# Kernel tuning notes

Hardware: AMD Instinct MI355X
Metric: run time of the kernel (lower is better)

Reference implementation:

```python
import jax, jax.numpy as jnp
import numpy as np

DIM = 2048
NUM_HEADS = 16
HEAD_DIM = DIM // NUM_HEADS
ROPE_BASE = 10000.0


def _rope_cos_sin(seq_len, head_dim, dtype):
    inv_freq = 1.0 / (ROPE_BASE ** (jnp.arange(0, head_dim, 2, dtype=jnp.float32) / head_dim))
    t = jnp.arange(seq_len, dtype=jnp.float32)
    freqs = jnp.einsum('i,j->ij', t, inv_freq)            # (T, head_dim/2)
    emb = jnp.concatenate([freqs, freqs], axis=-1)        # (T, head_dim)
    return jnp.cos(emb).astype(dtype), jnp.sin(emb).astype(dtype)


def _rotate_half(x):
    x1, x2 = jnp.split(x, 2, axis=-1)
    return jnp.concatenate([-x2, x1], axis=-1)


def setup_inputs() -> dict:
    key = jax.random.key(0)
    k1, k2, k3 = jax.random.split(key, 3)
    B, T = 2, 2048
    x = jax.random.normal(k1, (B, T, DIM), dtype=jnp.float32)
    # scale weights like nn.Linear default init (~1/sqrt(fan_in))
    w_qkv = jax.random.normal(k2, (DIM, 3 * DIM), dtype=jnp.float32) / np.sqrt(DIM)
    w_out = jax.random.normal(k3, (DIM, DIM), dtype=jnp.float32) / np.sqrt(DIM)
    return {"x": x, "w_qkv": w_qkv, "w_out": w_out}


def reference(x, w_qkv, w_out):
    B, T, D = x.shape
    H, Hd = NUM_HEADS, HEAD_DIM
    scale = Hd ** -0.5

    qkv = x @ w_qkv                                        # (B, T, 3D)
    q, k, v = jnp.split(qkv, 3, axis=-1)
    # (B, H, T, Hd)
    q = q.reshape(B, T, H, Hd).transpose(0, 2, 1, 3)
    k = k.reshape(B, T, H, Hd).transpose(0, 2, 1, 3)
    v = v.reshape(B, T, H, Hd).transpose(0, 2, 1, 3)

    cos, sin = _rope_cos_sin(T, Hd, x.dtype)               # (T, Hd)
    q = q * cos + _rotate_half(q) * sin
    k = k * cos + _rotate_half(k) * sin

    scores = jnp.einsum('bhqd,bhkd->bhqk', q, k) * scale   # (B, H, T, T)
    causal = jnp.tril(jnp.ones((T, T), dtype=bool))
    scores = jnp.where(causal[None, None, :, :], scores, jnp.float32(-jnp.inf))
    attn = jax.nn.softmax(scores, axis=-1)

    out = jnp.einsum('bhqk,bhkd->bhqd', attn, v)           # (B, H, T, Hd)
    out = out.transpose(0, 2, 1, 3).reshape(B, T, D)
    return out @ w_out
```

## Files before the change

kernel.cpp:

```cpp
#include <hip/hip_runtime.h>

typedef __attribute__((ext_vector_type(8))) short bf16x8;
typedef __attribute__((ext_vector_type(4))) float f32x4;

#define DEVICE __device__ __forceinline__

static constexpr int Tc = 2048;
static constexpr int Dc = 2048;
static constexpr int Hc = 16;
static constexpr int HD = 128;
static constexpr int MR = 4096;
static constexpr int NQKV = 6144;

DEVICE float bf2f(unsigned short u) {
  unsigned int t = ((unsigned int)u) << 16;
  float f; __builtin_memcpy(&f, &t, 4); return f;
}
DEVICE unsigned short f2bf(float f) {
  unsigned int t; __builtin_memcpy(&t, &f, 4);
  unsigned int r = (t + 0x7fffu + ((t >> 16) & 1u)) >> 16;
  return (unsigned short)r;
}

DEVICE void async_cp16(const void* g, void* lds) {
  __builtin_amdgcn_global_load_lds((const __attribute__((address_space(1))) void*)g,
                                   (__attribute__((address_space(3))) void*)lds, 16, 0, 0);
}

DEVICE int lsw(int t, int d2) {
  return t * 256 + (d2 ^ ((((t & 7) ^ ((t >> 3) & 7)) << 4)));
}

__global__ void rope_table_kernel(float2* cs) {
  int t = blockIdx.x;
  int j = threadIdx.x;
  float inv = powf(10000.0f, -(float)(2 * j) / 128.0f);
  float ang = (float)t * inv;
  cs[t * 64 + j] = make_float2(cosf(ang), sinf(ang));
}

__global__ void f32_to_bf16_kernel(const float* __restrict__ in,
                                   unsigned short* __restrict__ out, int n) {
  int i = (blockIdx.x * blockDim.x + threadIdx.x) * 4;
  if (i >= n) return;
  float4 v = *(const float4*)(in + i);
  ushort4 o;
  o.x = f2bf(v.x); o.y = f2bf(v.y); o.z = f2bf(v.z); o.w = f2bf(v.w);
  *(ushort4*)(out + i) = o;
}

__global__ __launch_bounds__(256)
void transpose_f32_bf16_kernel(const float* __restrict__ in,
                               unsigned short* __restrict__ out,
                               int R, int C) {
  __shared__ float tile[64][68];
  int c0 = blockIdx.x * 64, r0 = blockIdx.y * 64;
  int tid = threadIdx.x;
#pragma unroll
  for (int it = 0; it < 4; ++it) {
    int idx = it * 256 + tid;
    int r = idx >> 4;
    int c = (idx & 15) * 4;
    float4 v = *(const float4*)&in[(size_t)(r0 + r) * C + c0 + c];
    tile[r][c] = v.x; tile[r][c + 1] = v.y;
    tile[r][c + 2] = v.z; tile[r][c + 3] = v.w;
  }
  __syncthreads();
#pragma unroll
  for (int it = 0; it < 2; ++it) {
    int idx = it * 256 + tid;
    int r = idx >> 3;
    int c = (idx & 7) * 8;
    bf16x8 ov;
#pragma unroll
    for (int i = 0; i < 8; ++i) ov[i] = (short)f2bf(tile[c + i][r]);
    *(bf16x8*)&out[(size_t)(c0 + r) * R + r0 + c] = ov;
  }
}

__global__ __launch_bounds__(256, 2)
void gemm_qkv_kernel(const unsigned short* __restrict__ A,
                     const unsigned short* __restrict__ Bt,
                     const float2* __restrict__ cs,
                     unsigned short* __restrict__ qh,
                     unsigned short* __restrict__ kh,
                     unsigned short* __restrict__ vt) {
  const int N = NQKV, K = Dc;
  __shared__ __align__(16) unsigned short sh[128 * 128];
  unsigned short* As = sh;
  unsigned short* Bs = sh + 128 * 64;

  int nbx = N >> 7;
  int nwg = gridDim.x;
  int wg = blockIdx.x;
  int cpx = nwg >> 3;
  wg = (wg & 7) * cpx + (wg >> 3);
  int gsize = nbx * 8;
  int g = wg / gsize, rem = wg - g * gsize;
  int by = g * 8 + (rem & 7), bx = rem >> 3;
  int m0 = by << 7, n0 = bx << 7;

  int tid = threadIdx.x, lane = tid & 63, wid = tid >> 6;
  int wm = (wid >> 1) << 6, wn = (wid & 1) << 6;

  f32x4 acc[4][4] = {};

  for (int k0 = 0; k0 < K; k0 += 64) {
    __syncthreads();
#pragma unroll
    for (int r = 0; r < 4; ++r) {
      int p = r * 4096 + wid * 1024 + lane * 16;
      int row = p >> 7;
      int cb = (p & 127) ^ ((row & 7) << 4);
      const char* ga = (const char*)A + ((size_t)(m0 + row) * K + k0) * 2 + cb;
      async_cp16(ga, (char*)As + r * 4096 + wid * 1024);
      const char* gb = (const char*)Bt + ((size_t)(n0 + row) * K + k0) * 2 + cb;
      async_cp16(gb, (char*)Bs + r * 4096 + wid * 1024);
    }
    __syncthreads();

#pragma unroll
    for (int ks = 0; ks < 2; ++ks) {
      bf16x8 af[4], bfr[4];
#pragma unroll
      for (int mi = 0; mi < 4; ++mi) {
        int row = wm + mi * 16 + (lane & 15);
        int cb = (ks * 64 + ((lane >> 4) << 4)) ^ ((row & 7) << 4);
        af[mi] = *(const bf16x8*)((const char*)As + row * 128 + cb);
      }
#pragma unroll
      for (int ni = 0; ni < 4; ++ni) {
        int row = wn + ni * 16 + (lane & 15);
        int cb = (ks * 64 + ((lane >> 4) << 4)) ^ ((row & 7) << 4);
        bfr[ni] = *(const bf16x8*)((const char*)Bs + row * 128 + cb);
      }
#pragma unroll
      for (int mi = 0; mi < 4; ++mi)
#pragma unroll
        for (int ni = 0; ni < 4; ++ni)
          acc[mi][ni] = __builtin_amdgcn_mfma_f32_16x16x32_bf16(
              af[mi], bfr[ni], acc[mi][ni], 0, 0, 0);
    }
  }

  __syncthreads();
#pragma unroll
  for (int mi = 0; mi < 4; ++mi)
#pragma unroll
    for (int ni = 0; ni < 4; ++ni)
#pragma unroll
      for (int r = 0; r < 4; ++r) {
        int t_ = wm + mi * 16 + ((lane >> 4) << 2) + r;
        int d_ = wn + ni * 16 + (lane & 15);
        *(unsigned short*)((char*)sh + lsw(t_, d_ * 2)) = f2bf(acc[mi][ni][r]);
      }
  __syncthreads();

  int sector = n0 >> 11;
  int h = (n0 & 2047) >> 7;
  if (sector < 2) {
    unsigned short* dst = sector ? kh : qh;
#pragma unroll
    for (int it = 0; it < 4; ++it) {
      int idx = it * 256 + tid;
      int r = idx >> 3, j0 = (idx & 7) * 8;
      int m = m0 + r;
      int t = m & (Tc - 1), b = m >> 11;
      bf16x8 o1, o2;
#pragma unroll
      for (int i = 0; i < 8; ++i) {
        float q1 = bf2f(*(const unsigned short*)((const char*)sh + lsw(r, (j0 + i) * 2)));
        float q2 = bf2f(*(const unsigned short*)((const char*)sh + lsw(r, (j0 + i + 64) * 2)));
        float2 c = cs[t * 64 + j0 + i];
        o1[i] = (short)f2bf(q1 * c.x - q2 * c.y);
        o2[i] = (short)f2bf(q2 * c.x + q1 * c.y);
      }
      size_t ob = ((size_t)(b * Hc + h) * Tc + t) * HD;
      *(bf16x8*)(dst + ob + j0) = o1;
      *(bf16x8*)(dst + ob + 64 + j0) = o2;
    }
  } else {
    int bh = (m0 >> 11) * Hc + h;
    int tb = m0 & (Tc - 1);
#pragma unroll
    for (int it = 0; it < 8; ++it) {
      int idx = it * 256 + tid;
      int d = idx >> 4, tc = idx & 15;
      bf16x8 o;
#pragma unroll
      for (int i = 0; i < 8; ++i)
        o[i] = (short)*(const unsigned short*)((const char*)sh + lsw(tc * 8 + i, d * 2));
      *(bf16x8*)(vt + (size_t)(bh * HD + d) * Tc + tb + tc * 8) = o;
    }
  }
}

__global__ __launch_bounds__(256, 2)
void gemm_bt_kernel(const unsigned short* __restrict__ A,
                    const unsigned short* __restrict__ Bt,
                    float* __restrict__ C, int M, int N, int K) {
  __shared__ unsigned short As[128 * 64];
  __shared__ unsigned short Bs[128 * 64];

  int nbx = N >> 7;
  int nwg = gridDim.x;
  int wg = blockIdx.x;
  int cpx = nwg >> 3;
  wg = (wg & 7) * cpx + (wg >> 3);
  int gsize = nbx * 8;
  int g = wg / gsize, rem = wg - g * gsize;
  int by = g * 8 + (rem & 7), bx = rem >> 3;
  int m0 = by << 7, n0 = bx << 7;

  int tid = threadIdx.x, lane = tid & 63, wid = tid >> 6;
  int wm = (wid >> 1) << 6, wn = (wid & 1) << 6;

  f32x4 acc[4][4] = {};

  for (int k0 = 0; k0 < K; k0 += 64) {
    __syncthreads();
#pragma unroll
    for (int r = 0; r < 4; ++r) {
      int p = r * 4096 + wid * 1024 + lane * 16;
      int row = p >> 7;
      int cb = (p & 127) ^ ((row & 7) << 4);
      const char* ga = (const char*)A + ((size_t)(m0 + row) * K + k0) * 2 + cb;
      async_cp16(ga, (char*)As + r * 4096 + wid * 1024);
      const char* gb = (const char*)Bt + ((size_t)(n0 + row) * K + k0) * 2 + cb;
      async_cp16(gb, (char*)Bs + r * 4096 + wid * 1024);
    }
    __syncthreads();

#pragma unroll
    for (int ks = 0; ks < 2; ++ks) {
      bf16x8 af[4], bfr[4];
#pragma unroll
      for (int mi = 0; mi < 4; ++mi) {
        int row = wm + mi * 16 + (lane & 15);
        int cb = (ks * 64 + ((lane >> 4) << 4)) ^ ((row & 7) << 4);
        af[mi] = *(const bf16x8*)((const char*)As + row * 128 + cb);
      }
#pragma unroll
      for (int ni = 0; ni < 4; ++ni) {
        int row = wn + ni * 16 + (lane & 15);
        int cb = (ks * 64 + ((lane >> 4) << 4)) ^ ((row & 7) << 4);
        bfr[ni] = *(const bf16x8*)((const char*)Bs + row * 128 + cb);
      }
#pragma unroll
      for (int mi = 0; mi < 4; ++mi)
#pragma unroll
        for (int ni = 0; ni < 4; ++ni)
          acc[mi][ni] = __builtin_amdgcn_mfma_f32_16x16x32_bf16(
              af[mi], bfr[ni], acc[mi][ni], 0, 0, 0);
    }
  }

#pragma unroll
  for (int mi = 0; mi < 4; ++mi)
#pragma unroll
    for (int ni = 0; ni < 4; ++ni)
#pragma unroll
      for (int r = 0; r < 4; ++r) {
        int row = m0 + wm + mi * 16 + ((lane >> 4) << 2) + r;
        int col = n0 + wn + ni * 16 + (lane & 15);
        C[(size_t)row * N + col] = acc[mi][ni][r];
      }
}

__global__ __launch_bounds__(512, 1)
void attn_kernel(const unsigned short* __restrict__ qh,
                 const unsigned short* __restrict__ kh,
                 const unsigned short* __restrict__ vt,
                 unsigned short* __restrict__ ao) {
  const float SCL2 = 0.08838834764831845f * 1.4426950408889634f;
  int bh = blockIdx.x;
  int pairp = blockIdx.y;
  int b = bh >> 4, h = bh & 15;

  __shared__ unsigned short Ks[3][64 * 128];
  __shared__ unsigned short Vs[3][128 * 64];
  __shared__ unsigned short Ps[8][16 * 64];

  int tid = threadIdx.x, lane = tid & 63, wid = tid >> 6;

  const unsigned short* Kg = kh + (size_t)bh * Tc * HD;
  const unsigned short* Vg = vt + (size_t)bh * HD * Tc;

  auto stage = [&](int kt, int buf) {
#pragma unroll
    for (int r = 0; r < 2; ++r) {
      int p = r * 8192 + wid * 1024 + lane * 16;
      {
        int row = p >> 8, cb = p & 255;
        const char* g = (const char*)Kg + ((size_t)(kt * 64 + row)) * 256 +
                        (cb ^ ((row & 7) << 4));
        async_cp16(g, (char*)&Ks[buf][0] + r * 8192 + wid * 1024);
      }
      {
        int d = p >> 7, cb = p & 127;
        const char* g = (const char*)Vg + (size_t)d * (Tc * 2) + kt * 128 +
                        (cb ^ ((d & 7) << 4));
        async_cp16(g, (char*)&Vs[buf][0] + r * 8192 + wid * 1024);
      }
    }
  };

#pragma unroll 1
  for (int pass = 0; pass < 2; ++pass) {
    int qt = pass ? (15 - pairp) : pairp;
    const unsigned short* Qg = qh + ((size_t)bh * Tc + qt * 128) * HD;

    bf16x8 qf[4];
#pragma unroll
    for (int ks = 0; ks < 4; ++ks) {
      int row = wid * 16 + (lane & 15);
      qf[ks] = *(const bf16x8*)((const char*)Qg + row * 256 + ks * 64 +
                                ((lane >> 4) << 4));
    }
    asm volatile("s_waitcnt vmcnt(0)" ::: "memory");

    f32x4 oacc[8] = {};
    float mrow[4], lrow[4];
#pragma unroll
    for (int r = 0; r < 4; ++r) { mrow[r] = -1e30f; lrow[r] = 0.f; }

    int nkt = 2 * (qt + 1);
    __syncthreads();
    stage(0, 0);
    stage(1, 1);
#pragma unroll 1
    for (int kt = 0; kt < nkt; ++kt) {
      if (kt + 1 < nkt)
        asm volatile("s_waitcnt vmcnt(4)" ::: "memory");
      else
        asm volatile("s_waitcnt vmcnt(0)" ::: "memory");
      asm volatile("s_barrier" ::: "memory");
      if (kt + 2 < nkt) stage(kt + 2, (kt + 2) % 3);
      int cur = kt % 3;

      f32x4 sacc[4] = {};
      __builtin_amdgcn_s_setprio(1);
#pragma unroll
      for (int ks = 0; ks < 4; ++ks) {
#pragma unroll
        for (int ni = 0; ni < 4; ++ni) {
          int row = ni * 16 + (lane & 15);
          int cb = (ks * 64 + ((lane >> 4) << 4)) ^ ((row & 7) << 4);
          bf16x8 kf = *(const bf16x8*)((const char*)&Ks[cur][0] + row * 256 + cb);
          sacc[ni] = __builtin_amdgcn_mfma_f32_16x16x32_bf16(qf[ks], kf,
                                                             sacc[ni], 0, 0, 0);
        }
      }
      __builtin_amdgcn_s_setprio(0);

      bool diag = (kt >= 2 * qt);
      float sv[4][4];
      float pmax[4];
      bool allok = true;
#pragma unroll
      for (int r = 0; r < 4; ++r) {
        int qrow = qt * 128 + wid * 16 + ((lane >> 4) << 2) + r;
        float mx = -1e30f;
#pragma unroll
        for (int ni = 0; ni < 4; ++ni) {
          float s = sacc[ni][r] * SCL2;
          if (diag) {
            int kcol = kt * 64 + ni * 16 + (lane & 15);
            if (kcol > qrow) s = -1e30f;
          }
          sv[ni][r] = s;
          mx = fmaxf(mx, s);
        }
        pmax[r] = mx;
        allok = allok && (mx <= mrow[r] + 8.f);
      }
      if (!__all(allok)) {
#pragma unroll
        for (int r = 0; r < 4; ++r) {
          float gm = pmax[r];
          gm = fmaxf(gm, __shfl_xor(gm, 1));
          gm = fmaxf(gm, __shfl_xor(gm, 2));
          gm = fmaxf(gm, __shfl_xor(gm, 4));
          gm = fmaxf(gm, __shfl_xor(gm, 8));
          float mnew = fmaxf(mrow[r], gm);
          float fsc = exp2f(mrow[r] - mnew);
          mrow[r] = mnew;
          lrow[r] *= fsc;
#pragma unroll
          for (int nj = 0; nj < 8; ++nj) oacc[nj][r] *= fsc;
        }
      }

#pragma unroll
      for (int ni = 0; ni < 4; ++ni)
#pragma unroll
        for (int r = 0; r < 4; ++r) {
          float pp = exp2f(sv[ni][r] - mrow[r]);
          lrow[r] += pp;
          int row = ((lane >> 4) << 2) + r;
          int colb = (ni * 16 + (lane & 15)) * 2;
          *(unsigned short*)((char*)&Ps[wid][0] + row * 128 +
                             (colb ^ ((row & 7) << 4))) = f2bf(pp);
        }

      __builtin_amdgcn_s_setprio(1);
#pragma unroll
      for (int ks = 0; ks < 2; ++ks) {
        int prow = lane & 15;
        int pcb = (ks * 64 + ((lane >> 4) << 4)) ^ ((prow & 7) << 4);
        bf16x8 pf = *(const bf16x8*)((const char*)&Ps[wid][0] + prow * 128 + pcb);
#pragma unroll
        for (int nj = 0; nj < 8; ++nj) {
          int vrow = nj * 16 + (lane & 15);
          int vcb = (ks * 64 + ((lane >> 4) << 4)) ^ ((vrow & 7) << 4);
          bf16x8 vf = *(const bf16x8*)((const char*)&Vs[cur][0] + vrow * 128 + vcb);
          oacc[nj] = __builtin_amdgcn_mfma_f32_16x16x32_bf16(pf, vf,
                                                             oacc[nj], 0, 0, 0);
        }
      }
      __builtin_amdgcn_s_setprio(0);
    }

    float inv[4];
#pragma unroll
    for (int r = 0; r < 4; ++r) {
      float s = lrow[r];
      s += __shfl_xor(s, 1);
      s += __shfl_xor(s, 2);
      s += __shfl_xor(s, 4);
      s += __shfl_xor(s, 8);
      inv[r] = 1.f / s;
    }
#pragma unroll
    for (int nj = 0; nj < 8; ++nj)
#pragma unroll
      for (int r = 0; r < 4; ++r) {
        int trow = qt * 128 + wid * 16 + ((lane >> 4) << 2) + r;
        int col = nj * 16 + (lane & 15);
        ao[((size_t)(b * Tc + trow)) * Dc + h * HD + col] =
            f2bf(oacc[nj][r] * inv[r]);
      }
  }
}

extern "C" void kernel_launch(void* const* d_in, const int* in_sizes, int n_in,
                              void* d_out, int out_size, void* d_ws,
                              size_t ws_size, hipStream_t stream) {
  const float* x = (const float*)d_in[0];
  const float* w_qkv = (const float*)d_in[1];
  const float* w_out = (const float*)d_in[2];
  float* out = (float*)d_out;

  char* ws = (char*)d_ws;
  size_t off = 0;
  auto alloc = [&](size_t bytes) {
    char* p = ws + off;
    off += (bytes + 255) & ~(size_t)255;
    return p;
  };
  unsigned short* xb    = (unsigned short*)alloc((size_t)MR * Dc * 2);
  unsigned short* wqkvT = (unsigned short*)alloc((size_t)NQKV * Dc * 2);
  unsigned short* woutT = (unsigned short*)alloc((size_t)Dc * Dc * 2);
  unsigned short* qhp   = (unsigned short*)alloc((size_t)MR * Dc * 2);
  unsigned short* khp   = (unsigned short*)alloc((size_t)MR * Dc * 2);
  unsigned short* vtp   = (unsigned short*)alloc((size_t)MR * Dc * 2);
  unsigned short* aop   = (unsigned short*)alloc((size_t)MR * Dc * 2);
  float2* cs            = (float2*)alloc((size_t)Tc * 64 * sizeof(float2));

  rope_table_kernel<<<Tc, 64, 0, stream>>>(cs);
  f32_to_bf16_kernel<<<(MR * Dc / 4 + 255) / 256, 256, 0, stream>>>(x, xb, MR * Dc);
  transpose_f32_bf16_kernel<<<dim3(NQKV / 64, Dc / 64), 256, 0, stream>>>(
      w_qkv, wqkvT, Dc, NQKV);
  transpose_f32_bf16_kernel<<<dim3(Dc / 64, Dc / 64), 256, 0, stream>>>(
      w_out, woutT, Dc, Dc);
  gemm_qkv_kernel<<<(MR / 128) * (NQKV / 128), 256, 0, stream>>>(
      xb, wqkvT, cs, qhp, khp, vtp);
  attn_kernel<<<dim3(32, 8), 512, 0, stream>>>(qhp, khp, vtp, aop);
  gemm_bt_kernel<<<(MR / 128) * (Dc / 128), 256, 0, stream>>>(
      aop, woutT, out, MR, Dc, Dc);
}
```

Baseline: 250.3 us.

## Halve attention block to 4 waves, each handling 32 query rows

Cuts the attention kernel from 8 to 4 waves per block. Each wave now computes two 16-row query sub-tiles, so every K and V fragment read from LDS feeds two MFMAs instead of one. Staging loops are rewritten so 256 threads cover the same K/V tiles, and the wait count is raised to match the larger number of in-flight copies. This lowers LDS read traffic per MFMA, at the cost of fewer waves to hide latency and roughly double the accumulator registers per thread.

Result: slower. 279.1 us (+11.5%).

```diff
diff --git a/kernel.cpp b/kernel.cpp
--- a/kernel.cpp
+++ b/kernel.cpp
@@ -267,7 +267,7 @@
       }
 }
 
-__global__ __launch_bounds__(512, 1)
+__global__ __launch_bounds__(256, 1)
 void attn_kernel(const unsigned short* __restrict__ qh,
                  const unsigned short* __restrict__ kh,
                  const unsigned short* __restrict__ vt,
@@ -279,7 +279,7 @@
 
   __shared__ unsigned short Ks[3][64 * 128];
   __shared__ unsigned short Vs[3][128 * 64];
-  __shared__ unsigned short Ps[8][16 * 64];
+  __shared__ unsigned short Ps[4][32 * 64];
 
   int tid = threadIdx.x, lane = tid & 63, wid = tid >> 6;
 
@@ -288,19 +288,19 @@
 
   auto stage = [&](int kt, int buf) {
 #pragma unroll
-    for (int r = 0; r < 2; ++r) {
-      int p = r * 8192 + wid * 1024 + lane * 16;
+    for (int r = 0; r < 4; ++r) {
+      int p = r * 4096 + tid * 16;
       {
         int row = p >> 8, cb = p & 255;
         const char* g = (const char*)Kg + ((size_t)(kt * 64 + row)) * 256 +
                         (cb ^ ((row & 7) << 4));
-        async_cp16(g, (char*)&Ks[buf][0] + r * 8192 + wid * 1024);
+        async_cp16(g, (char*)&Ks[buf][0] + (p & ~15));
       }
       {
         int d = p >> 7, cb = p & 127;
         const char* g = (const char*)Vg + (size_t)d * (Tc * 2) + kt * 128 +
                         (cb ^ ((d & 7) << 4));
-        async_cp16(g, (char*)&Vs[buf][0] + r * 8192 + wid * 1024);
+        async_cp16(g, (char*)&Vs[buf][0] + (p & ~15));
       }
     }
   };
@@ -310,19 +310,23 @@
     int qt = pass ? (15 - pairp) : pairp;
     const unsigned short* Qg = qh + ((size_t)bh * Tc + qt * 128) * HD;
 
-    bf16x8 qf[4];
-#pragma unroll
-    for (int ks = 0; ks < 4; ++ks) {
-      int row = wid * 16 + (lane & 15);
-      qf[ks] = *(const bf16x8*)((const char*)Qg + row * 256 + ks * 64 +
-                                ((lane >> 4) << 4));
-    }
+    bf16x8 qf[2][4];
+#pragma unroll
+    for (int mi = 0; mi < 2; ++mi)
+#pragma unroll
+      for (int ks = 0; ks < 4; ++ks) {
+        int row = wid * 32 + mi * 16 + (lane & 15);
+        qf[mi][ks] = *(const bf16x8*)((const char*)Qg + row * 256 + ks * 64 +
+                                      ((lane >> 4) << 4));
+      }
     asm volatile("s_waitcnt vmcnt(0)" ::: "memory");
 
-    f32x4 oacc[8] = {};
-    float mrow[4], lrow[4];
-#pragma unroll
-    for (int r = 0; r < 4; ++r) { mrow[r] = -1e30f; lrow[r] = 0.f; }
+    f32x4 oacc[2][8] = {};
+    float mrow[2][4], lrow[2][4];
+#pragma unroll
+    for (int mi = 0; mi < 2; ++mi)
+#pragma unroll
+      for (int r = 0; r < 4; ++r) { mrow[mi][r] = -1e30f; lrow[mi][r] = 0.f; }
 
     int nkt = 2 * (qt + 1);
     __syncthreads();
@@ -331,14 +335,14 @@
 #pragma unroll 1
     for (int kt = 0; kt < nkt; ++kt) {
       if (kt + 1 < nkt)
-        asm volatile("s_waitcnt vmcnt(4)" ::: "memory");
+        asm volatile("s_waitcnt vmcnt(8)" ::: "memory");
       else
         asm volatile("s_waitcnt vmcnt(0)" ::: "memory");
       asm volatile("s_barrier" ::: "memory");
       if (kt + 2 < nkt) stage(kt + 2, (kt + 2) % 3);
       int cur = kt % 3;
 
-      f32x4 sacc[4] = {};
+      f32x4 sacc[2][4] = {};
       __builtin_amdgcn_s_setprio(1);
 #pragma unroll
       for (int ks = 0; ks < 4; ++ks) {
@@ -347,99 +351,116 @@
           int row = ni * 16 + (lane & 15);
           int cb = (ks * 64 + ((lane >> 4) << 4)) ^ ((row & 7) << 4);
           bf16x8 kf = *(const bf16x8*)((const char*)&Ks[cur][0] + row * 256 + cb);
-          sacc[ni] = __builtin_amdgcn_mfma_f32_16x16x32_bf16(qf[ks], kf,
-                                                             sacc[ni], 0, 0, 0);
+#pragma unroll
+          for (int mi = 0; mi < 2; ++mi)
+            sacc[mi][ni] = __builtin_amdgcn_mfma_f32_16x16x32_bf16(
+                qf[mi][ks], kf, sacc[mi][ni], 0, 0, 0);
         }
       }
       __builtin_amdgcn_s_setprio(0);
 
       bool diag = (kt >= 2 * qt);
-      float sv[4][4];
-      float pmax[4];
+      float sv[2][4][4];
+      float pmax[2][4];
       bool allok = true;
 #pragma unroll
-      for (int r = 0; r < 4; ++r) {
-        int qrow = qt * 128 + wid * 16 + ((lane >> 4) << 2) + r;
-        float mx = -1e30f;
-#pragma unroll
-        for (int ni = 0; ni < 4; ++ni) {
-          float s = sacc[ni][r] * SCL2;
-          if (diag) {
-            int kcol = kt * 64 + ni * 16 + (lane & 15);
-            if (kcol > qrow) s = -1e30f;
+      for (int mi = 0; mi < 2; ++mi)
+#pragma unroll
+        for (int r = 0; r < 4; ++r) {
+          int qrow = qt * 128 + wid * 32 + mi * 16 + ((lane >> 4) << 2) + r;
+          float mx = -1e30f;
+#pragma unroll
+          for (int ni = 0; ni < 4; ++ni) {
+            float s = sacc[mi][ni][r] * SCL2;
+            if (diag) {
+              int kcol = kt * 64 + ni * 16 + (lane & 15);
+              if (kcol > qrow) s = -1e30f;
+            }
+            sv[mi][ni][r] = s;
+            mx = fmaxf(mx, s);
           }
-          sv[ni][r] = s;
-          mx = fmaxf(mx, s);
+          pmax[mi][r] = mx;
+          allok = allok && (mx <= mrow[mi][r] + 8.f);
         }
-        pmax[r] = mx;
-        allok = allok && (mx <= mrow[r] + 8.f);
-      }
       if (!__all(allok)) {
 #pragma unroll
-        for (int r = 0; r < 4; ++r) {
-          float gm = pmax[r];
-          gm = fmaxf(gm, __shfl_xor(gm, 1));
-          gm = fmaxf(gm, __shfl_xor(gm, 2));
-          gm = fmaxf(gm, __shfl_xor(gm, 4));
-          gm = fmaxf(gm, __shfl_xor(gm, 8));
-          float mnew = fmaxf(mrow[r], gm);
-          float fsc = exp2f(mrow[r] - mnew);
-          mrow[r] = mnew;
-          lrow[r] *= fsc;
-#pragma unroll
-          for (int nj = 0; nj < 8; ++nj) oacc[nj][r] *= fsc;
+        for (int mi = 0; mi < 2; ++mi)
+#pragma unroll
+          for (int r = 0; r < 4; ++r) {
+            float gm = pmax[mi][r];
+            gm = fmaxf(gm, __shfl_xor(gm, 1));
+            gm = fmaxf(gm, __shfl_xor(gm, 2));
+            gm = fmaxf(gm, __shfl_xor(gm, 4));
+            gm = fmaxf(gm, __shfl_xor(gm, 8));
+            float mnew = fmaxf(mrow[mi][r], gm);
+            float fsc = exp2f(mrow[mi][r] - mnew);
+            mrow[mi][r] = mnew;
+            lrow[mi][r] *= fsc;
+#pragma unroll
+            for (int nj = 0; nj < 8; ++nj) oacc[mi][nj][r] *= fsc;
+          }
+      }
+
+#pragma unroll
+      for (int mi = 0; mi < 2; ++mi)
+#pragma unroll
+        for (int ni = 0; ni < 4; ++ni)
+#pragma unroll
+          for (int r = 0; r < 4; ++r) {
+            float pp = exp2f(sv[mi][ni][r] - mrow[mi][r]);
+            lrow[mi][r] += pp;
+            int row = mi * 16 + ((lane >> 4) << 2) + r;
+            int colb = (ni * 16 + (lane & 15)) * 2;
+            *(unsigned short*)((char*)&Ps[wid][0] + row * 128 +
+                               (colb ^ ((row & 7) << 4))) = f2bf(pp);
+          }
+
+      __builtin_amdgcn_s_setprio(1);
+#pragma unroll
+      for (int ks = 0; ks < 2; ++ks) {
+        bf16x8 pf[2];
+#pragma unroll
+        for (int mi = 0; mi < 2; ++mi) {
+          int prow = mi * 16 + (lane & 15);
+          int pcb = (ks * 64 + ((lane >> 4) << 4)) ^ ((prow & 7) << 4);
+          pf[mi] = *(const bf16x8*)((const char*)&Ps[wid][0] + prow * 128 + pcb);
         }
-      }
-
-#pragma unroll
-      for (int ni = 0; ni < 4; ++ni)
-#pragma unroll
-        for (int r = 0; r < 4; ++r) {
-          float pp = exp2f(sv[ni][r] - mrow[r]);
-          lrow[r] += pp;
-          int row = ((lane >> 4) << 2) + r;
-          int colb = (ni * 16 + (lane & 15)) * 2;
-          *(unsigned short*)((char*)&Ps[wid][0] + row * 128 +
-                             (colb ^ ((row & 7) << 4))) = f2bf(pp);
-        }
-
-      __builtin_amdgcn_s_setprio(1);
-#pragma unroll
-      for (int ks = 0; ks < 2; ++ks) {
-        int prow = lane & 15;
-        int pcb = (ks * 64 + ((lane >> 4) << 4)) ^ ((prow & 7) << 4);
-        bf16x8 pf = *(const bf16x8*)((const char*)&Ps[wid][0] + prow * 128 + pcb);
 #pragma unroll
         for (int nj = 0; nj < 8; ++nj) {
           int vrow = nj * 16 + (lane & 15);
           int vcb = (ks * 64 + ((lane >> 4) << 4)) ^ ((vrow & 7) << 4);
           bf16x8 vf = *(const bf16x8*)((const char*)&Vs[cur][0] + vrow * 128 + vcb);
-          oacc[nj] = __builtin_amdgcn_mfma_f32_16x16x32_bf16(pf, vf,
-                                                             oacc[nj], 0, 0, 0);
+#pragma unroll
+          for (int mi = 0; mi < 2; ++mi)
+            oacc[mi][nj] = __builtin_amdgcn_mfma_f32_16x16x32_bf16(
+                pf[mi], vf, oacc[mi][nj], 0, 0, 0);
         }
       }
       __builtin_amdgcn_s_setprio(0);
     }
 
-    float inv[4];
-#pragma unroll
-    for (int r = 0; r < 4; ++r) {
-      float s = lrow[r];
-      s += __shfl_xor(s, 1);
-      s += __shfl_xor(s, 2);
-      s += __shfl_xor(s, 4);
-      s += __shfl_xor(s, 8);
-      inv[r] = 1.f / s;
-    }
-#pragma unroll
-    for (int nj = 0; nj < 8; ++nj)
+#pragma unroll
+    for (int mi = 0; mi < 2; ++mi) {
+      float inv[4];
 #pragma unroll
       for (int r = 0; r < 4; ++r) {
-        int trow = qt * 128 + wid * 16 + ((lane >> 4) << 2) + r;
-        int col = nj * 16 + (lane & 15);
-        ao[((size_t)(b * Tc + trow)) * Dc + h * HD + col] =
-            f2bf(oacc[nj][r] * inv[r]);
-      }
+        float s = lrow[mi][r];
+        s += __shfl_xor(s, 1);
+        s += __shfl_xor(s, 2);
+        s += __shfl_xor(s, 4);
+        s += __shfl_xor(s, 8);
+        inv[r] = 1.f / s;
+      }
+#pragma unroll
+      for (int nj = 0; nj < 8; ++nj)
+#pragma unroll
+        for (int r = 0; r < 4; ++r) {
+          int trow = qt * 128 + wid * 32 + mi * 16 + ((lane >> 4) << 2) + r;
+          int col = nj * 16 + (lane & 15);
+          ao[((size_t)(b * Tc + trow)) * Dc + h * HD + col] =
+              f2bf(oacc[mi][nj][r] * inv[r]);
+        }
+    }
   }
 }
 
@@ -475,7 +496,7 @@
       w_out, woutT, Dc, Dc);
   gemm_qkv_kernel<<<(MR / 128) * (NQKV / 128), 256, 0, stream>>>(
       xb, wqkvT, cs, qhp, khp, vtp);
-  attn_kernel<<<dim3(32, 8), 512, 0, stream>>>(qhp, khp, vtp, aop);
+  attn_kernel<<<dim3(32, 8), 256, 0, stream>>>(qhp, khp, vtp, aop);
   gemm_bt_kernel<<<(MR / 128) * (Dc / 128), 256, 0, stream>>>(
       aop, woutT, out, MR, Dc, Dc);
 }
```

## Double-buffer LDS tiles in QKV and output GEMMs to overlap loads with MFMA

Applied to the files above, without the earlier changes.

Both bf16 GEMM kernels now keep two LDS buffers for the A and B tiles and issue the async global-to-LDS copies for the next K tile before computing on the current one. They wait with s_waitcnt vmcnt(8) so only the previous stage's copies must land. The intent is to hide global memory latency behind MFMA work instead of stalling at each barrier. LDS use doubles to 64 KB per block, which may limit occupancy at 2 blocks per CU, and the hand-written waitcnt/barrier sequence depends on the exact count of outstanding loads.

After: 253.3 us. Within noise of the previous version (+1.2%).

```diff
diff --git a/kernel.cpp b/kernel.cpp
--- a/kernel.cpp
+++ b/kernel.cpp
@@ -86,9 +86,7 @@
                      unsigned short* __restrict__ kh,
                      unsigned short* __restrict__ vt) {
   const int N = NQKV, K = Dc;
-  __shared__ __align__(16) unsigned short sh[128 * 128];
-  unsigned short* As = sh;
-  unsigned short* Bs = sh + 128 * 64;
+  __shared__ __align__(16) unsigned short sh[4 * 128 * 64];
 
   int nbx = N >> 7;
   int nwg = gridDim.x;
@@ -105,19 +103,34 @@
 
   f32x4 acc[4][4] = {};
 
-  for (int k0 = 0; k0 < K; k0 += 64) {
-    __syncthreads();
+  auto stage = [&](int kt, int buf) {
+    int k0 = kt << 6;
 #pragma unroll
     for (int r = 0; r < 4; ++r) {
       int p = r * 4096 + wid * 1024 + lane * 16;
       int row = p >> 7;
       int cb = (p & 127) ^ ((row & 7) << 4);
       const char* ga = (const char*)A + ((size_t)(m0 + row) * K + k0) * 2 + cb;
-      async_cp16(ga, (char*)As + r * 4096 + wid * 1024);
+      async_cp16(ga, (char*)(sh + buf * 8192) + r * 4096 + wid * 1024);
       const char* gb = (const char*)Bt + ((size_t)(n0 + row) * K + k0) * 2 + cb;
-      async_cp16(gb, (char*)Bs + r * 4096 + wid * 1024);
-    }
-    __syncthreads();
+      async_cp16(gb, (char*)(sh + 16384 + buf * 8192) + r * 4096 + wid * 1024);
+    }
+  };
+
+  int nkt = K >> 6;
+  stage(0, 0);
+#pragma unroll 1
+  for (int t = 0; t < nkt; ++t) {
+    asm volatile("s_barrier" ::: "memory");
+    if (t + 1 < nkt) {
+      stage(t + 1, (t + 1) & 1);
+      asm volatile("s_waitcnt vmcnt(8)" ::: "memory");
+    } else {
+      asm volatile("s_waitcnt vmcnt(0)" ::: "memory");
+    }
+    asm volatile("s_barrier" ::: "memory");
+    const char* Ab = (const char*)(sh + (t & 1) * 8192);
+    const char* Bb = (const char*)(sh + 16384 + (t & 1) * 8192);
 
 #pragma unroll
     for (int ks = 0; ks < 2; ++ks) {
@@ -126,13 +139,13 @@
       for (int mi = 0; mi < 4; ++mi) {
         int row = wm + mi * 16 + (lane & 15);
         int cb = (ks * 64 + ((lane >> 4) << 4)) ^ ((row & 7) << 4);
-        af[mi] = *(const bf16x8*)((const char*)As + row * 128 + cb);
+        af[mi] = *(const bf16x8*)(Ab + row * 128 + cb);
       }
 #pragma unroll
       for (int ni = 0; ni < 4; ++ni) {
         int row = wn + ni * 16 + (lane & 15);
         int cb = (ks * 64 + ((lane >> 4) << 4)) ^ ((row & 7) << 4);
-        bfr[ni] = *(const bf16x8*)((const char*)Bs + row * 128 + cb);
+        bfr[ni] = *(const bf16x8*)(Bb + row * 128 + cb);
       }
 #pragma unroll
       for (int mi = 0; mi < 4; ++mi)
@@ -199,8 +212,8 @@
 void gemm_bt_kernel(const unsigned short* __restrict__ A,
                     const unsigned short* __restrict__ Bt,
                     float* __restrict__ C, int M, int N, int K) {
-  __shared__ unsigned short As[128 * 64];
-  __shared__ unsigned short Bs[128 * 64];
+  __shared__ __align__(16) unsigned short As[2][128 * 64];
+  __shared__ __align__(16) unsigned short Bs[2][128 * 64];
 
   int nbx = N >> 7;
   int nwg = gridDim.x;
@@ -217,19 +230,34 @@
 
   f32x4 acc[4][4] = {};
 
-  for (int k0 = 0; k0 < K; k0 += 64) {
-    __syncthreads();
+  auto stage = [&](int kt, int buf) {
+    int k0 = kt << 6;
 #pragma unroll
     for (int r = 0; r < 4; ++r) {
       int p = r * 4096 + wid * 1024 + lane * 16;
       int row = p >> 7;
       int cb = (p & 127) ^ ((row & 7) << 4);
       const char* ga = (const char*)A + ((size_t)(m0 + row) * K + k0) * 2 + cb;
-      async_cp16(ga, (char*)As + r * 4096 + wid * 1024);
+      async_cp16(ga, (char*)&As[buf][0] + r * 4096 + wid * 1024);
       const char* gb = (const char*)Bt + ((size_t)(n0 + row) * K + k0) * 2 + cb;
-      async_cp16(gb, (char*)Bs + r * 4096 + wid * 1024);
-    }
-    __syncthreads();
+      async_cp16(gb, (char*)&Bs[buf][0] + r * 4096 + wid * 1024);
+    }
+  };
+
+  int nkt = K >> 6;
+  stage(0, 0);
+#pragma unroll 1
+  for (int t = 0; t < nkt; ++t) {
+    asm volatile("s_barrier" ::: "memory");
+    if (t + 1 < nkt) {
+      stage(t + 1, (t + 1) & 1);
+      asm volatile("s_waitcnt vmcnt(8)" ::: "memory");
+    } else {
+      asm volatile("s_waitcnt vmcnt(0)" ::: "memory");
+    }
+    asm volatile("s_barrier" ::: "memory");
+    const char* Ab = (const char*)&As[t & 1][0];
+    const char* Bb = (const char*)&Bs[t & 1][0];
 
 #pragma unroll
     for (int ks = 0; ks < 2; ++ks) {
@@ -238,13 +266,13 @@
       for (int mi = 0; mi < 4; ++mi) {
         int row = wm + mi * 16 + (lane & 15);
         int cb = (ks * 64 + ((lane >> 4) << 4)) ^ ((row & 7) << 4);
-        af[mi] = *(const bf16x8*)((const char*)As + row * 128 + cb);
+        af[mi] = *(const bf16x8*)(Ab + row * 128 + cb);
       }
 #pragma unroll
       for (int ni = 0; ni < 4; ++ni) {
         int row = wn + ni * 16 + (lane & 15);
         int cb = (ks * 64 + ((lane >> 4) << 4)) ^ ((row & 7) << 4);
-        bfr[ni] = *(const bf16x8*)((const char*)Bs + row * 128 + cb);
+        bfr[ni] = *(const bf16x8*)(Bb + row * 128 + cb);
       }
 #pragma unroll
       for (int mi = 0; mi < 4; ++mi)
```
